# Kernel tuning notes

Measured on AMD Instinct MI355X. Metric: run time of the kernel, lower is better.

The kernel has to match this reference:

```python
import jax, jax.numpy as jnp
import numpy as np

D_IN = 1024
D_OUT = 1024
NUM_HEADS = 16
HEAD_DIM = D_OUT // NUM_HEADS


def setup_inputs() -> dict:
    key = jax.random.key(0)
    k1, k2, k3, k4 = jax.random.split(key, 4)
    x = jax.random.normal(k1, (2, 2048, D_IN), dtype=jnp.float32)
    # Linear weights stored torch-style [out_features, in_features]
    W_qkv = jax.random.normal(k2, (3 * D_OUT, D_IN), dtype=jnp.float32) * (1.0 / np.sqrt(D_IN))
    W_out = jax.random.normal(k3, (D_OUT, D_OUT), dtype=jnp.float32) * (1.0 / np.sqrt(D_OUT))
    b_out = jax.random.normal(k4, (D_OUT,), dtype=jnp.float32) * 0.01
    return {"x": x, "W_qkv": W_qkv, "W_out": W_out, "b_out": b_out}


def reference(x, W_qkv, W_out, b_out):
    b, s, _ = x.shape
    qkv = jnp.einsum('bsi,oi->bso', x, W_qkv)  # [b, s, 3*d_out]
    q, k, v = jnp.split(qkv, 3, axis=-1)
    def to_heads(t):
        return t.reshape(b, s, NUM_HEADS, HEAD_DIM).transpose(0, 2, 1, 3)
    q, k, v = to_heads(q), to_heads(k), to_heads(v)
    # NOTE: original module does NOT scale by 1/sqrt(head_dim)
    scores = jnp.einsum('bhqd,bhkd->bhqk', q, k)
    causal = jnp.tril(jnp.ones((s, s), dtype=bool))  # True = keep
    scores = jnp.where(causal[None, None], scores, -jnp.inf)
    attn = jax.nn.softmax(scores, axis=-1)
    ctx = jnp.einsum('bhqk,bhkd->bhqd', attn, v)
    ctx = ctx.transpose(0, 2, 1, 3).reshape(b, s, D_OUT)
    return jnp.einsum('bso,po->bsp', ctx, W_out) + b_out
```

## Files before the change

kernel.cpp:

```cpp
#include <hip/hip_runtime.h>
#include <cstdint>
#include <cstddef>


typedef __attribute__((ext_vector_type(8))) short bf16x8;
typedef __attribute__((ext_vector_type(4))) float f32x4;

#define LOG2E 1.44269504f

#define MFMA16(a, b, c) __builtin_amdgcn_mfma_f32_16x16x32_bf16((a), (b), (c), 0, 0, 0)

#define GLDS16(g, s)                                                        \
  __builtin_amdgcn_global_load_lds(                                         \
      (const __attribute__((address_space(1))) void*)(g),                   \
      (__attribute__((address_space(3))) void*)(s), 16, 0, 0)

#define ASYNC_BAR(N) asm volatile("s_waitcnt vmcnt(" #N ")\n\ts_barrier" ::: "memory")

#if __has_builtin(__builtin_amdgcn_exp2f)
#define EXP2F(x) __builtin_amdgcn_exp2f(x)
#else
#define EXP2F(x) exp2f(x)
#endif

static __device__ __forceinline__ unsigned short f2bf(float f) {
  unsigned int u = __builtin_bit_cast(unsigned int, f);
  u += 0x7FFFu + ((u >> 16) & 1u);
  return (unsigned short)(u >> 16);
}

static __device__ __forceinline__ unsigned int pk2bf(float a, float b) {
  const unsigned int ua = __builtin_bit_cast(unsigned int, a) + 0x8000u;
  const unsigned int ub = __builtin_bit_cast(unsigned int, b) + 0x8000u;
  return __builtin_amdgcn_perm(ub, ua, 0x07060302);
}

__global__ __launch_bounds__(256) void cast_bf16(const float* __restrict__ x,
                                                 const float* __restrict__ wq,
                                                 const float* __restrict__ wo,
                                                 unsigned short* __restrict__ xb,
                                                 unsigned short* __restrict__ wqb,
                                                 unsigned short* __restrict__ wob)
{
  const int id = blockIdx.x * 256 + threadIdx.x;
  const float* src;
  unsigned short* dst;
  int off;
  if (id < 1048576)               { src = x;  dst = xb;  off = id; }
  else if (id < 1048576 + 786432) { src = wq; dst = wqb; off = id - 1048576; }
  else                            { src = wo; dst = wob; off = id - (1048576 + 786432); }
  float4 v = ((const float4*)src)[off];
  ushort4 o;
  o.x = f2bf(v.x); o.y = f2bf(v.y); o.z = f2bf(v.z); o.w = f2bf(v.w);
  ((ushort4*)dst)[off] = o;
}

__global__ __launch_bounds__(256) void gemm_qkv(const unsigned short* __restrict__ A,
                                                const unsigned short* __restrict__ B,
                                                unsigned short* __restrict__ Qb,
                                                unsigned short* __restrict__ Kb,
                                                unsigned short* __restrict__ Vt)
{
  __shared__ unsigned short pool[24576];

  const int tid  = threadIdx.x;
  const int wave = tid >> 6, lane = tid & 63, quad = lane >> 4, cl = lane & 15;
  const int wm = wave >> 1, wn = wave & 1;
  const int m0 = blockIdx.y * 128, n0 = blockIdx.x * 128;
  const int sr = lane >> 2, sc = lane & 3;

  const int part = n0 >> 10;
  const bool swapped = (part < 2);

  f32x4 acc[4][4];
  #pragma unroll
  for (int i = 0; i < 4; ++i)
    #pragma unroll
    for (int j = 0; j < 4; ++j)
      #pragma unroll
      for (int r = 0; r < 4; ++r) acc[i][j][r] = 0.f;

  const int scs = (sc ^ ((sr >> 1) & 3)) * 8;
  const int rchunk = (quad ^ ((cl >> 1) & 3)) * 8;

  auto stage = [&](int k0, int buf) {
    unsigned short* As = pool + buf * 8192;
    unsigned short* Bs = As + 4096;
    #pragma unroll
    for (int ii = 0; ii < 2; ++ii) {
      const int r = wave * 32 + ii * 16 + sr;
      GLDS16(A + (size_t)(m0 + r) * 1024 + k0 + scs, &As[(wave * 32 + ii * 16) * 32]);
      GLDS16(B + (size_t)(n0 + r) * 1024 + k0 + scs, &Bs[(wave * 32 + ii * 16) * 32]);
    }
  };

  stage(0, 0);
  stage(32, 1);
  int cur = 0;
  #pragma unroll 1
  for (int it = 0; it < 32; ++it) {
    if (it + 2 < 32) {
      ASYNC_BAR(4);
      const int bnx = (cur == 0) ? 2 : cur - 1;
      stage((it + 2) * 32, bnx);
    } else if (it + 1 < 32) {
      ASYNC_BAR(4);
    } else {
      ASYNC_BAR(0);
    }

    const unsigned short* As = pool + cur * 8192;
    const unsigned short* Bs = As + 4096;
    bf16x8 af[4], bfr[4];
    #pragma unroll
    for (int mt = 0; mt < 4; ++mt)
      af[mt] = *(const bf16x8*)&As[(wm * 64 + mt * 16 + cl) * 32 + rchunk];
    #pragma unroll
    for (int nt = 0; nt < 4; ++nt)
      bfr[nt] = *(const bf16x8*)&Bs[(wn * 64 + nt * 16 + cl) * 32 + rchunk];

    if (swapped) {
      #pragma unroll
      for (int mt = 0; mt < 4; ++mt)
        #pragma unroll
        for (int nt = 0; nt < 4; ++nt)
          acc[mt][nt] = MFMA16(bfr[nt], af[mt], acc[mt][nt]);
    } else {
      #pragma unroll
      for (int mt = 0; mt < 4; ++mt)
        #pragma unroll
        for (int nt = 0; nt < 4; ++nt)
          acc[mt][nt] = MFMA16(af[mt], bfr[nt], acc[mt][nt]);
    }
    cur = (cur == 2) ? 0 : cur + 1;
  }

  const int bb = m0 >> 11, ss = m0 & 2047;
  if (part == 2) {
    #pragma unroll
    for (int half = 0; half < 2; ++half) {
      __syncthreads();
      if (wn == half) {
        #pragma unroll
        for (int mt = 0; mt < 4; ++mt)
          #pragma unroll
          for (int nt = 0; nt < 4; ++nt) {
            const int nl = nt * 16 + cl;
            const int ml = wm * 64 + mt * 16 + quad * 4;
            ushort4 pk;
            pk.x = f2bf(acc[mt][nt][0]); pk.y = f2bf(acc[mt][nt][1]);
            pk.z = f2bf(acc[mt][nt][2]); pk.w = f2bf(acc[mt][nt][3]);
            *(ushort4*)&pool[nl * 136 + ml] = pk;
          }
      }
      __syncthreads();
      const int row = tid >> 2, q4 = tid & 3;
      const int nglob = n0 + half * 64 + row;
      const int hh = (nglob >> 6) & 15, d = nglob & 63;
      unsigned short* drow = Vt + ((size_t)(bb * 16 + hh) * 64 + d) * 2048 + ss;
      #pragma unroll
      for (int i = 0; i < 4; ++i) {
        const bf16x8 v = *(const bf16x8*)&pool[row * 136 + q4 * 32 + i * 8];
        *(bf16x8*)(drow + q4 * 32 + i * 8) = v;
      }
    }
  } else {
    unsigned short* dst = (part == 0) ? Qb : Kb;
    const float sc2 = (part == 0) ? LOG2E : 1.0f;
    #pragma unroll
    for (int mt = 0; mt < 4; ++mt) {
      const int m = ss + wm * 64 + mt * 16 + cl;
      #pragma unroll
      for (int nt = 0; nt < 4; ++nt) {
        const int np = (n0 & 1023) + wn * 64 + nt * 16 + quad * 4;
        const int hh = np >> 6, d0 = np & 63;
        ushort4 pk;
        pk.x = f2bf(acc[mt][nt][0] * sc2);
        pk.y = f2bf(acc[mt][nt][1] * sc2);
        pk.z = f2bf(acc[mt][nt][2] * sc2);
        pk.w = f2bf(acc[mt][nt][3] * sc2);
        *(ushort4*)&dst[((size_t)(bb * 16 + hh) * 2048 + m) * 64 + d0] = pk;
      }
    }
  }
}

__global__ __launch_bounds__(256) void gemm_out(const unsigned short* __restrict__ A,
                                                const unsigned short* __restrict__ B,
                                                const float* __restrict__ bias,
                                                float* __restrict__ OutF)
{
  __shared__ unsigned short pool[18432];

  const int tid  = threadIdx.x;
  const int wave = tid >> 6, lane = tid & 63, quad = lane >> 4, cl = lane & 15;
  const int wm = wave >> 1, wn = wave & 1;
  const int m0 = blockIdx.y * 128, n0 = blockIdx.x * 64;
  const int sr = lane >> 2, sc = lane & 3;

  f32x4 acc[4][2];
  #pragma unroll
  for (int i = 0; i < 4; ++i)
    #pragma unroll
    for (int j = 0; j < 2; ++j)
      #pragma unroll
      for (int r = 0; r < 4; ++r) acc[i][j][r] = 0.f;

  const int scs = (sc ^ ((sr >> 1) & 3)) * 8;
  const int rchunk = (quad ^ ((cl >> 1) & 3)) * 8;

  auto stage = [&](int k0, int buf) {
    unsigned short* As = pool + buf * 6144;
    unsigned short* Bs = As + 4096;
    #pragma unroll
    for (int ii = 0; ii < 2; ++ii) {
      const int r = wave * 32 + ii * 16 + sr;
      GLDS16(A + (size_t)(m0 + r) * 1024 + k0 + scs, &As[(wave * 32 + ii * 16) * 32]);
    }
    const int rb = wave * 16 + sr;
    GLDS16(B + (size_t)(n0 + rb) * 1024 + k0 + scs, &Bs[wave * 16 * 32]);
  };

  stage(0, 0);
  stage(32, 1);
  int cur = 0;
  #pragma unroll 1
  for (int it = 0; it < 32; ++it) {
    if (it + 2 < 32) {
      ASYNC_BAR(3);
      const int bnx = (cur == 0) ? 2 : cur - 1;
      stage((it + 2) * 32, bnx);
    } else if (it + 1 < 32) {
      ASYNC_BAR(3);
    } else {
      ASYNC_BAR(0);
    }

    const unsigned short* As = pool + cur * 6144;
    const unsigned short* Bs = As + 4096;
    bf16x8 af[4], bfr[2];
    #pragma unroll
    for (int mt = 0; mt < 4; ++mt)
      af[mt] = *(const bf16x8*)&As[(wm * 64 + mt * 16 + cl) * 32 + rchunk];
    #pragma unroll
    for (int nt = 0; nt < 2; ++nt)
      bfr[nt] = *(const bf16x8*)&Bs[(wn * 32 + nt * 16 + cl) * 32 + rchunk];

    #pragma unroll
    for (int mt = 0; mt < 4; ++mt)
      #pragma unroll
      for (int nt = 0; nt < 2; ++nt)
        acc[mt][nt] = MFMA16(bfr[nt], af[mt], acc[mt][nt]);
    cur = (cur == 2) ? 0 : cur + 1;
  }

  #pragma unroll
  for (int mt = 0; mt < 4; ++mt) {
    const int m = m0 + wm * 64 + mt * 16 + cl;
    #pragma unroll
    for (int nt = 0; nt < 2; ++nt) {
      const int n = n0 + wn * 32 + nt * 16 + quad * 4;
      const float4 bv = *(const float4*)(bias + n);
      float4 o;
      o.x = acc[mt][nt][0] + bv.x; o.y = acc[mt][nt][1] + bv.y;
      o.z = acc[mt][nt][2] + bv.z; o.w = acc[mt][nt][3] + bv.w;
      *(float4*)&OutF[(size_t)m * 1024 + n] = o;
    }
  }
}

__global__ __launch_bounds__(256) void attn_mfma(const unsigned short* __restrict__ Qb,
                                                 const unsigned short* __restrict__ Kb,
                                                 const unsigned short* __restrict__ Vt,
                                                 unsigned short* __restrict__ CTX)
{
  __shared__ unsigned short Ksm[3][32 * 64];
  __shared__ unsigned short Vsm[3][64 * 32];
  __shared__ unsigned short Psm[4][32 * 40];

  const int tid  = threadIdx.x;
  const int wave = tid >> 6, lane = tid & 63, quad = lane >> 4, cl = lane & 15;

  const int L  = blockIdx.x;
  const int bh = 4 * (L & 7) + ((L >> 3) & 3);
  const int b  = bh >> 4, h = bh & 15;
  const int p  = L >> 5;
  const int g  = p * 4 + wave;
  const int qlo = g * 16;
  const int qhi = (127 - g) * 16;
  const size_t base = (size_t)bh * (2048 * 64);

  bf16x8 qf[2][2];
  #pragma unroll
  for (int dk = 0; dk < 2; ++dk) {
    qf[0][dk] = *(const bf16x8*)(Qb + base + (size_t)(qlo + cl) * 64 + dk * 32 + quad * 8);
    qf[1][dk] = *(const bf16x8*)(Qb + base + (size_t)(qhi + cl) * 64 + dk * 32 + quad * 8);
  }

  f32x4 oacc[2][4];
  #pragma unroll
  for (int mf = 0; mf < 2; ++mf)
    #pragma unroll
    for (int dt = 0; dt < 4; ++dt)
      #pragma unroll
      for (int r = 0; r < 4; ++r) oacc[mf][dt][r] = 0.f;
  float lr[2][4] = {};

  bf16x8 ones;
  #pragma unroll
  for (int k = 0; k < 8; ++k) ones[k] = (short)0x3F80;

  const int krow  = lane >> 3;
  const int kslot = (lane & 7) ^ krow;
  const int vrow  = lane >> 2;
  const int vslot = (lane & 3) ^ (vrow & 3);

  const int nch = 64 - 2 * p;

  auto stageKV = [&](int j32, int buf) {
    GLDS16(Kb + base + (size_t)(j32 + wave * 8 + krow) * 64 + kslot * 8,
           &Ksm[buf][wave * 8 * 64]);
    GLDS16(Vt + base + (size_t)(wave * 16 + vrow) * 2048 + j32 + vslot * 8,
           &Vsm[buf][wave * 16 * 32]);
  };

  stageKV(0, 0);
  stageKV(32, 1);
  int cur = 0;
  #pragma unroll 1
  for (int ch = 0; ch < nch; ++ch) {
    if (ch + 2 < nch) {
      ASYNC_BAR(2);
      const int bnx = (cur == 0) ? 2 : cur - 1;
      stageKV((ch + 2) * 32, bnx);
    } else if (ch + 1 < nch) {
      ASYNC_BAR(2);
    } else {
      ASYNC_BAR(0);
    }

    const int jg0 = ch * 32;
    if (jg0 <= qhi + 15) {
      const bool lowAct = (jg0 <= qlo + 15);

      bf16x8 kf[2][2];
      #pragma unroll
      for (int jf = 0; jf < 2; ++jf)
        #pragma unroll
        for (int dk = 0; dk < 2; ++dk) {
          const int slot = (dk * 4 + quad) ^ (cl & 7);
          kf[jf][dk] = *(const bf16x8*)&Ksm[cur][(jf * 16 + cl) * 64 + slot * 8];
        }

      f32x4 st[2][2];
      #pragma unroll
      for (int jf = 0; jf < 2; ++jf)
        #pragma unroll
        for (int mf = 0; mf < 2; ++mf) {
          if (mf == 0 && !lowAct) continue;
          f32x4 z;
          #pragma unroll
          for (int r = 0; r < 4; ++r) z[r] = 0.f;
          z = MFMA16(kf[jf][0], qf[mf][0], z);
          st[jf][mf] = MFMA16(kf[jf][1], qf[mf][1], z);
        }

      #pragma unroll
      for (int mf = 0; mf < 2; ++mf) {
        if (mf == 0 && !lowAct) continue;
        const int qbase = mf ? qhi : qlo;
        const bool diag = (jg0 + 32 > qbase);
        #pragma unroll
        for (int jf = 0; jf < 2; ++jf) {
          float pv[4];
          if (diag) {
            const int qg = qbase + cl;
            #pragma unroll
            for (int r = 0; r < 4; ++r) {
              const int jg = jg0 + jf * 16 + quad * 4 + r;
              pv[r] = (jg <= qg) ? EXP2F(st[jf][mf][r]) : 0.f;
            }
          } else {
            #pragma unroll
            for (int r = 0; r < 4; ++r) pv[r] = EXP2F(st[jf][mf][r]);
          }
          uint2 w;
          w.x = pk2bf(pv[0], pv[1]);
          w.y = pk2bf(pv[2], pv[3]);
          *(uint2*)&Psm[wave][(mf * 16 + cl) * 40 + jf * 16 + quad * 4] = w;
        }
      }

      bf16x8 vf[4];
      #pragma unroll
      for (int dt = 0; dt < 4; ++dt) {
        const int d = dt * 16 + cl;
        const int slot = quad ^ (cl & 3);
        vf[dt] = *(const bf16x8*)&Vsm[cur][d * 32 + slot * 8];
      }

      #pragma unroll
      for (int mf = 0; mf < 2; ++mf) {
        if (mf == 0 && !lowAct) continue;
        const bf16x8 pf = *(const bf16x8*)&Psm[wave][(mf * 16 + cl) * 40 + quad * 8];
        f32x4 z;
        #pragma unroll
        for (int r = 0; r < 4; ++r) z[r] = 0.f;
        const f32x4 ls = MFMA16(pf, ones, z);
        #pragma unroll
        for (int r = 0; r < 4; ++r) lr[mf][r] += ls[r];
        #pragma unroll
        for (int dt = 0; dt < 4; ++dt)
          oacc[mf][dt] = MFMA16(pf, vf[dt], oacc[mf][dt]);
      }
    }
    cur = (cur == 2) ? 0 : cur + 1;
  }

  #pragma unroll
  for (int mf = 0; mf < 2; ++mf) {
    const int qbase = mf ? qhi : qlo;
    float inv[4];
    #pragma unroll
    for (int r = 0; r < 4; ++r) inv[r] = 1.f / lr[mf][r];
    #pragma unroll
    for (int dt = 0; dt < 4; ++dt)
      #pragma unroll
      for (int r = 0; r < 4; ++r)
        CTX[(size_t)(b * 2048 + qbase + quad * 4 + r) * 1024 +
            h * 64 + dt * 16 + cl] = f2bf(oacc[mf][dt][r] * inv[r]);
  }
}

extern "C" void kernel_launch(void* const* d_in, const int* in_sizes, int n_in,
                              void* d_out, int out_size, void* d_ws, size_t ws_size,
                              hipStream_t stream)
{
  const float* x    = (const float*)d_in[0];
  const float* Wqkv = (const float*)d_in[1];
  const float* Wout = (const float*)d_in[2];
  const float* bout = (const float*)d_in[3];
  float* out = (float*)d_out;

  char* ws = (char*)d_ws;
  unsigned short* xb  = (unsigned short*)(ws);
  unsigned short* wqb = (unsigned short*)(ws + 8388608);
  unsigned short* wob = (unsigned short*)(ws + 14680064);
  unsigned short* Qb  = (unsigned short*)(ws + 16777216);
  unsigned short* Kb  = (unsigned short*)(ws + 25165824);
  unsigned short* Vt  = (unsigned short*)(ws + 33554432);
  unsigned short* CTX = (unsigned short*)(ws + 41943040);

  cast_bf16<<<dim3(8192), dim3(256), 0, stream>>>(x, Wqkv, Wout, xb, wqb, wob);

  gemm_qkv<<<dim3(24, 32), dim3(256), 0, stream>>>(xb, wqb, Qb, Kb, Vt);

  attn_mfma<<<dim3(512), dim3(256), 0, stream>>>(Qb, Kb, Vt, CTX);

  gemm_out<<<dim3(16, 32), dim3(256), 0, stream>>>(CTX, wob, bout, out);
}
```

Before: 209.3 us.

## Remap GEMM blocks for XCD locality and double attention KV chunk size

Both GEMM kernels move to a 1D grid and remap block indices so that blocks placed on the same XCD (round-robin by block index mod 8) share N-columns of the weight, which should improve L2 reuse. The attention kernel now stages 64-key K/V chunks per pipeline step instead of 32. This halves the number of barriers and loop iterations, at the cost of more LDS per block (48KB K/V triple buffers), which may reduce occupancy. The V layout in LDS gets a wider swizzle to match.

```diff
diff --git a/kernel.cpp b/kernel.cpp
--- a/kernel.cpp
+++ b/kernel.cpp
@@ -66,7 +66,12 @@
   const int tid  = threadIdx.x;
   const int wave = tid >> 6, lane = tid & 63, quad = lane >> 4, cl = lane & 15;
   const int wm = wave >> 1, wn = wave & 1;
-  const int m0 = blockIdx.y * 128, n0 = blockIdx.x * 128;
+
+  const int L = blockIdx.x;
+  const int xcd = L & 7, s = L >> 3;
+  const int j = 3 * xcd + (s % 3);
+  const int i = s / 3;
+  const int m0 = i * 128, n0 = j * 128;
   const int sr = lane >> 2, sc = lane & 3;
 
   const int part = n0 >> 10;
@@ -74,11 +79,11 @@
 
   f32x4 acc[4][4];
   #pragma unroll
-  for (int i = 0; i < 4; ++i)
-    #pragma unroll
-    for (int j = 0; j < 4; ++j)
-      #pragma unroll
-      for (int r = 0; r < 4; ++r) acc[i][j][r] = 0.f;
+  for (int a = 0; a < 4; ++a)
+    #pragma unroll
+    for (int b2 = 0; b2 < 4; ++b2)
+      #pragma unroll
+      for (int r = 0; r < 4; ++r) acc[a][b2][r] = 0.f;
 
   const int scs = (sc ^ ((sr >> 1) & 3)) * 8;
   const int rchunk = (quad ^ ((cl >> 1) & 3)) * 8;
@@ -159,9 +164,9 @@
       const int hh = (nglob >> 6) & 15, d = nglob & 63;
       unsigned short* drow = Vt + ((size_t)(bb * 16 + hh) * 64 + d) * 2048 + ss;
       #pragma unroll
-      for (int i = 0; i < 4; ++i) {
-        const bf16x8 v = *(const bf16x8*)&pool[row * 136 + q4 * 32 + i * 8];
-        *(bf16x8*)(drow + q4 * 32 + i * 8) = v;
+      for (int k = 0; k < 4; ++k) {
+        const bf16x8 v = *(const bf16x8*)&pool[row * 136 + q4 * 32 + k * 8];
+        *(bf16x8*)(drow + q4 * 32 + k * 8) = v;
       }
     }
   } else {
@@ -195,16 +200,21 @@
   const int tid  = threadIdx.x;
   const int wave = tid >> 6, lane = tid & 63, quad = lane >> 4, cl = lane & 15;
   const int wm = wave >> 1, wn = wave & 1;
-  const int m0 = blockIdx.y * 128, n0 = blockIdx.x * 64;
+
+  const int L = blockIdx.x;
+  const int xcd = L & 7, s = L >> 3;
+  const int j = 2 * xcd + (s & 1);
+  const int i = s >> 1;
+  const int m0 = i * 128, n0 = j * 64;
   const int sr = lane >> 2, sc = lane & 3;
 
   f32x4 acc[4][2];
   #pragma unroll
-  for (int i = 0; i < 4; ++i)
-    #pragma unroll
-    for (int j = 0; j < 2; ++j)
-      #pragma unroll
-      for (int r = 0; r < 4; ++r) acc[i][j][r] = 0.f;
+  for (int a = 0; a < 4; ++a)
+    #pragma unroll
+    for (int b2 = 0; b2 < 2; ++b2)
+      #pragma unroll
+      for (int r = 0; r < 4; ++r) acc[a][b2][r] = 0.f;
 
   const int scs = (sc ^ ((sr >> 1) & 3)) * 8;
   const int rchunk = (quad ^ ((cl >> 1) & 3)) * 8;
@@ -274,8 +284,8 @@
                                                  const unsigned short* __restrict__ Vt,
                                                  unsigned short* __restrict__ CTX)
 {
-  __shared__ unsigned short Ksm[3][32 * 64];
-  __shared__ unsigned short Vsm[3][64 * 32];
+  __shared__ unsigned short Ksm[3][64 * 64];
+  __shared__ unsigned short Vsm[3][64 * 64];
   __shared__ unsigned short Psm[4][32 * 40];
 
   const int tid  = threadIdx.x;
@@ -310,46 +320,50 @@
   #pragma unroll
   for (int k = 0; k < 8; ++k) ones[k] = (short)0x3F80;
 
-  const int krow  = lane >> 3;
-  const int kslot = (lane & 7) ^ krow;
-  const int vrow  = lane >> 2;
-  const int vslot = (lane & 3) ^ (vrow & 3);
-
-  const int nch = 64 - 2 * p;
-
-  auto stageKV = [&](int j32, int buf) {
-    GLDS16(Kb + base + (size_t)(j32 + wave * 8 + krow) * 64 + kslot * 8,
-           &Ksm[buf][wave * 8 * 64]);
-    GLDS16(Vt + base + (size_t)(wave * 16 + vrow) * 2048 + j32 + vslot * 8,
-           &Vsm[buf][wave * 16 * 32]);
+  const int lrow  = lane >> 3;
+  const int lslot = (lane & 7) ^ lrow;
+  const int nch = 32 - p;
+
+  auto stageKV = [&](int j64, int buf) {
+    #pragma unroll
+    for (int ii = 0; ii < 2; ++ii) {
+      const int r0 = wave * 16 + ii * 8;
+      GLDS16(Kb + base + (size_t)(j64 + r0 + lrow) * 64 + lslot * 8, &Ksm[buf][r0 * 64]);
+      GLDS16(Vt + base + (size_t)(r0 + lrow) * 2048 + j64 + lslot * 8, &Vsm[buf][r0 * 64]);
+    }
   };
 
   stageKV(0, 0);
-  stageKV(32, 1);
+  stageKV(64, 1);
   int cur = 0;
   #pragma unroll 1
   for (int ch = 0; ch < nch; ++ch) {
     if (ch + 2 < nch) {
-      ASYNC_BAR(2);
+      ASYNC_BAR(4);
       const int bnx = (cur == 0) ? 2 : cur - 1;
-      stageKV((ch + 2) * 32, bnx);
+      stageKV((ch + 2) * 64, bnx);
     } else if (ch + 1 < nch) {
-      ASYNC_BAR(2);
+      ASYNC_BAR(4);
     } else {
       ASYNC_BAR(0);
     }
 
-    const int jg0 = ch * 32;
-    if (jg0 <= qhi + 15) {
+    const int j64 = ch * 64;
+    #pragma unroll
+    for (int jli = 0; jli < 2; ++jli) {
+      const int jg0 = j64 + jli * 32;
+      if (jg0 > qhi + 15) continue;
       const bool lowAct = (jg0 <= qlo + 15);
+      const int jl = jli * 32;
 
       bf16x8 kf[2][2];
       #pragma unroll
       for (int jf = 0; jf < 2; ++jf)
         #pragma unroll
         for (int dk = 0; dk < 2; ++dk) {
+          const int jrow = jl + jf * 16 + cl;
           const int slot = (dk * 4 + quad) ^ (cl & 7);
-          kf[jf][dk] = *(const bf16x8*)&Ksm[cur][(jf * 16 + cl) * 64 + slot * 8];
+          kf[jf][dk] = *(const bf16x8*)&Ksm[cur][jrow * 64 + slot * 8];
         }
 
       f32x4 st[2][2];
@@ -395,8 +409,8 @@
       #pragma unroll
       for (int dt = 0; dt < 4; ++dt) {
         const int d = dt * 16 + cl;
-        const int slot = quad ^ (cl & 3);
-        vf[dt] = *(const bf16x8*)&Vsm[cur][d * 32 + slot * 8];
+        const int slot = ((jl >> 3) + quad) ^ (cl & 7);
+        vf[dt] = *(const bf16x8*)&Vsm[cur][d * 64 + slot * 8];
       }
 
       #pragma unroll
@@ -453,9 +467,9 @@
 
   cast_bf16<<<dim3(8192), dim3(256), 0, stream>>>(x, Wqkv, Wout, xb, wqb, wob);
 
-  gemm_qkv<<<dim3(24, 32), dim3(256), 0, stream>>>(xb, wqb, Qb, Kb, Vt);
+  gemm_qkv<<<dim3(768), dim3(256), 0, stream>>>(xb, wqb, Qb, Kb, Vt);
 
   attn_mfma<<<dim3(512), dim3(256), 0, stream>>>(Qb, Kb, Vt, CTX);
 
-  gemm_out<<<dim3(16, 32), dim3(256), 0, stream>>>(CTX, wob, bout, out);
-}
+  gemm_out<<<dim3(512), dim3(256), 0, stream>>>(CTX, wob, bout, out);
+}
```

Result: faster. 201.1 us (-3.9%).
